# Performance work log

Hardware: AMD Instinct MI355X
Metric: run time of the kernel (lower is better)

## Reference

```python
import jax, jax.numpy as jnp
import numpy as np

BOUNDS = 1.6  # aabb = [[b,b,b],[-b,-b,-b]]
C = 72       # output_coordinate_dim per plane


def _sample_planes(grids, coords):
    """Bilinear grid_sample, align_corners=True, padding_mode='border'.
    grids:  [P, C, H, W]
    coords: [P, N, 2] with (x, y) in [-1, 1]; x indexes W, y indexes H.
    returns [P, N, C]
    """
    P, Cc, H, W = grids.shape
    x = (coords[..., 0] + 1.0) * 0.5 * (W - 1)
    y = (coords[..., 1] + 1.0) * 0.5 * (H - 1)
    # border padding: clamp the sampling coordinate to the valid range
    x = jnp.clip(x, 0.0, W - 1)
    y = jnp.clip(y, 0.0, H - 1)
    x0 = jnp.floor(x)
    y0 = jnp.floor(y)
    wx = (x - x0)[..., None]  # [P, N, 1]
    wy = (y - y0)[..., None]
    x0i = x0.astype(jnp.int32)
    y0i = y0.astype(jnp.int32)
    x1i = jnp.minimum(x0i + 1, W - 1)
    y1i = jnp.minimum(y0i + 1, H - 1)

    def one_plane(g, y0i, y1i, x0i, x1i):
        # g: [C, H, W]; index tensors: [N] -> each gather [C, N] -> [N, C]
        v00 = g[:, y0i, x0i].T
        v01 = g[:, y0i, x1i].T
        v10 = g[:, y1i, x0i].T
        v11 = g[:, y1i, x1i].T
        return v00, v01, v10, v11

    v00, v01, v10, v11 = jax.vmap(one_plane)(grids, y0i, y1i, x0i, x1i)
    top = v00 * (1.0 - wx) + v01 * wx
    bot = v10 * (1.0 - wx) + v11 * wx
    return top * (1.0 - wy) + bot * wy  # [P, N, C]


def _triplane_forward(pts, grids_list):
    N = pts.shape[0]
    # normalize_aabb with aabb = [[b,b,b],[-b,-b,-b]]
    pts_n = (pts - BOUNDS) * (2.0 / (-BOUNDS - BOUNDS)) - 1.0  # == -pts / BOUNDS
    # plane coordinate combos: (0,1), (0,2), (1,2)
    coords = jnp.stack([pts_n[:, jnp.array([0, 1])],
                        pts_n[:, jnp.array([0, 2])],
                        pts_n[:, jnp.array([1, 2])]], axis=0)  # [3, N, 2]
    feats = []
    prev = None
    for g in grids_list:  # fixed small loop over scales
        samp = _sample_planes(g, coords)                 # [3, N, C]
        tri = samp.transpose(1, 0, 2).reshape(N, 3 * C)  # concat plane feats
        prev = tri if prev is None else tri + prev       # cumulative across scales
        feats.append(prev)
    return jnp.concatenate(feats, axis=-1)  # [N, 3*C*n_scales]


def setup_inputs() -> dict:
    key = jax.random.key(0)
    ks = jax.random.split(key, 5)
    N = 100000
    pts = jax.random.normal(ks[0], (N, 3), dtype=jnp.float32)
    resos = [64, 128, 256, 512]
    grids = {}
    for i, r in enumerate(resos):
        # original init is uniform(-0.01, 0.01)
        grids[f"grids_s{i}"] = jax.random.uniform(
            ks[i + 1], (3, C, r, r), dtype=jnp.float32, minval=-0.01, maxval=0.01)
    return {"pts": pts, **grids}


def reference(pts, grids_s0, grids_s1, grids_s2, grids_s3):
    return _triplane_forward(pts, [grids_s0, grids_s1, grids_s2, grids_s3])
```

## Files before the change

kernel.cpp:

```cpp
#include <hip/hip_runtime.h>


#define TP_C 72
#define TP_PLANES 3
#define TP_SCALES 4
#define TP_INV_BOUNDS 0.625f
#define TP_CVEC (TP_C / 4)

__global__ __launch_bounds__(256) void transpose_kernel(
    const float* __restrict__ in, float* __restrict__ out, int r)
{
    __shared__ float tile[32][33];

    int xt = blockIdx.x * 32;
    int ct = blockIdx.y * 32;
    int py = blockIdx.z;
    int p  = py / r;
    int y  = py - p * r;
    int tx = threadIdx.x;
    int ty = threadIdx.y;

    const float* inp = in + ((size_t)p * TP_C) * (size_t)r * (size_t)r + (size_t)y * r;

    #pragma unroll
    for (int i = 0; i < 4; ++i) {
        int c = ct + ty + i * 8;
        if (c < TP_C) {
            tile[ty + i * 8][tx] = inp[(size_t)c * r * r + xt + tx];
        }
    }
    __syncthreads();

    float* outp = out + ((size_t)py * r) * TP_C;
    #pragma unroll
    for (int i = 0; i < 4; ++i) {
        int x = xt + ty + i * 8;
        int c = ct + tx;
        if (c < TP_C) {
            outp[(size_t)x * TP_C + c] = tile[tx][ty + i * 8];
        }
    }
}

__global__ __launch_bounds__(256) void triplane_gather_kernel(
    const float* __restrict__ pts,
    const float* __restrict__ t0,
    const float* __restrict__ t1,
    const float* __restrict__ t2,
    const float* __restrict__ t3,
    float* __restrict__ out,
    int N)
{
    int idx = blockIdx.x * blockDim.x + threadIdx.x;
    int total = N * TP_PLANES * TP_CVEC;
    if (idx >= total) return;

    int cv = idx % TP_CVEC;
    int t  = idx / TP_CVEC;
    int p  = t % TP_PLANES;
    int n  = t / TP_PLANES;

    float nx = -pts[n * 3 + 0] * TP_INV_BOUNDS;
    float ny = -pts[n * 3 + 1] * TP_INV_BOUNDS;
    float nz = -pts[n * 3 + 2] * TP_INV_BOUNDS;

    float cx, cy;
    if (p == 0)      { cx = nx; cy = ny; }
    else if (p == 1) { cx = nx; cy = nz; }
    else             { cx = ny; cy = nz; }

    const float* grids[TP_SCALES] = { t0, t1, t2, t3 };
    const int    res[TP_SCALES]   = { 64, 128, 256, 512 };

    float4 acc = make_float4(0.f, 0.f, 0.f, 0.f);
    float* outrow = out + (size_t)n * (TP_SCALES * TP_PLANES * TP_C)
                        + (size_t)p * TP_C + cv * 4;

    #pragma unroll
    for (int s = 0; s < TP_SCALES; ++s) {
        const int r = res[s];
        const float rm1 = (float)(r - 1);

        float fx = (cx + 1.0f) * 0.5f * rm1;
        float fy = (cy + 1.0f) * 0.5f * rm1;
        fx = fminf(fmaxf(fx, 0.0f), rm1);
        fy = fminf(fmaxf(fy, 0.0f), rm1);

        float x0f = floorf(fx);
        float y0f = floorf(fy);
        float wx = fx - x0f;
        float wy = fy - y0f;
        int x0 = (int)x0f;
        int y0 = (int)y0f;
        int x1 = min(x0 + 1, r - 1);
        int y1 = min(y0 + 1, r - 1);

        const float* g = grids[s] + ((size_t)p * r * r) * TP_C + (size_t)cv * 4;
        const float4* r0c0 = (const float4*)(g + ((size_t)y0 * r + x0) * TP_C);
        const float4* r0c1 = (const float4*)(g + ((size_t)y0 * r + x1) * TP_C);
        const float4* r1c0 = (const float4*)(g + ((size_t)y1 * r + x0) * TP_C);
        const float4* r1c1 = (const float4*)(g + ((size_t)y1 * r + x1) * TP_C);

        float4 v00 = *r0c0;
        float4 v01 = *r0c1;
        float4 v10 = *r1c0;
        float4 v11 = *r1c1;

        float iwx = 1.0f - wx;
        float iwy = 1.0f - wy;

        float tpx, tpy, tpz, tpw, bt;
        tpx = v00.x * iwx + v01.x * wx;
        bt  = v10.x * iwx + v11.x * wx;
        acc.x += tpx * iwy + bt * wy;
        tpy = v00.y * iwx + v01.y * wx;
        bt  = v10.y * iwx + v11.y * wx;
        acc.y += tpy * iwy + bt * wy;
        tpz = v00.z * iwx + v01.z * wx;
        bt  = v10.z * iwx + v11.z * wx;
        acc.z += tpz * iwy + bt * wy;
        tpw = v00.w * iwx + v01.w * wx;
        bt  = v10.w * iwx + v11.w * wx;
        acc.w += tpw * iwy + bt * wy;

        *(float4*)(outrow + s * (TP_PLANES * TP_C)) = acc;
    }
}

extern "C" void kernel_launch(void* const* d_in, const int* in_sizes, int n_in,
                              void* d_out, int out_size, void* d_ws, size_t ws_size,
                              hipStream_t stream) {
    const float* pts = (const float*)d_in[0];
    const float* g[TP_SCALES] = {
        (const float*)d_in[1], (const float*)d_in[2],
        (const float*)d_in[3], (const float*)d_in[4] };
    float* out = (float*)d_out;

    const int res[TP_SCALES] = { 64, 128, 256, 512 };

    float* tg[TP_SCALES];
    size_t off = 0;
    for (int s = 0; s < TP_SCALES; ++s) {
        tg[s] = (float*)d_ws + off;
        off += (size_t)TP_PLANES * TP_C * res[s] * res[s];
    }

    for (int s = 0; s < TP_SCALES; ++s) {
        int r = res[s];
        dim3 block(32, 8);
        dim3 grid(r / 32, (TP_C + 31) / 32, TP_PLANES * r);
        transpose_kernel<<<grid, block, 0, stream>>>(g[s], tg[s], r);
    }

    int N = in_sizes[0] / 3;
    int total = N * TP_PLANES * TP_CVEC;
    int block = 256;
    int grid = (total + block - 1) / block;
    triplane_gather_kernel<<<grid, block, 0, stream>>>(
        pts, tg[0], tg[1], tg[2], tg[3], out, N);
}
```

Baseline: 821.9 us.

## Merge per-scale grid transposes into one launch with float4 wide tiles

Replaces four separate transpose launches with a single kernel whose blocks index into a concatenated tile space across all scales. Each block transposes 128 pixels by 72 channels through padded shared memory, reading float4 along pixels and writing float4 contiguous channel-last rows. This is meant to cut launch overhead, the wasted threads from padding 72 channels to 96, and the narrow scalar global accesses. The larger shared-memory tile (about 37KB) may lower occupancy, and the float4 loads rely on pixel offsets staying 16-byte aligned.

```diff
diff --git a/kernel.cpp b/kernel.cpp
--- a/kernel.cpp
+++ b/kernel.cpp
@@ -7,38 +7,59 @@
 #define TP_INV_BOUNDS 0.625f
 #define TP_CVEC (TP_C / 4)
 
-__global__ __launch_bounds__(256) void transpose_kernel(
-    const float* __restrict__ in, float* __restrict__ out, int r)
+#define TP_TILES0 96
+#define TP_TILES1 480
+#define TP_TILES2 2016
+#define TP_TILES3 8160
+
+__global__ __launch_bounds__(256) void transpose_all_kernel(
+    const float* __restrict__ g0, const float* __restrict__ g1,
+    const float* __restrict__ g2, const float* __restrict__ g3,
+    float* __restrict__ t0, float* __restrict__ t1,
+    float* __restrict__ t2, float* __restrict__ t3)
 {
-    __shared__ float tile[32][33];
+    int b = blockIdx.x;
+    const float* in;
+    float* out;
+    int rr, tile;
+    if (b < TP_TILES0)      { in = g0; out = t0; rr = 64 * 64;   tile = b; }
+    else if (b < TP_TILES1) { in = g1; out = t1; rr = 128 * 128; tile = b - TP_TILES0; }
+    else if (b < TP_TILES2) { in = g2; out = t2; rr = 256 * 256; tile = b - TP_TILES1; }
+    else                    { in = g3; out = t3; rr = 512 * 512; tile = b - TP_TILES2; }
 
-    int xt = blockIdx.x * 32;
-    int ct = blockIdx.y * 32;
-    int py = blockIdx.z;
-    int p  = py / r;
-    int y  = py - p * r;
-    int tx = threadIdx.x;
-    int ty = threadIdx.y;
+    int P0  = tile * 128;
+    int p   = P0 / rr;
+    int px0 = P0 - p * rr;
 
-    const float* inp = in + ((size_t)p * TP_C) * (size_t)r * (size_t)r + (size_t)y * r;
+    __shared__ float lds[TP_C * 129];
+
+    const float* inp = in + ((size_t)p * TP_C) * (size_t)rr + px0;
+    int t = threadIdx.x;
 
     #pragma unroll
-    for (int i = 0; i < 4; ++i) {
-        int c = ct + ty + i * 8;
-        if (c < TP_C) {
-            tile[ty + i * 8][tx] = inp[(size_t)c * r * r + xt + tx];
-        }
+    for (int j = 0; j < 9; ++j) {
+        int idx = j * 256 + t;
+        int c   = idx >> 5;
+        int q4  = idx & 31;
+        float4 v = *(const float4*)(inp + (size_t)c * rr + q4 * 4);
+        float* l = lds + c * 129 + q4 * 4;
+        l[0] = v.x; l[1] = v.y; l[2] = v.z; l[3] = v.w;
     }
     __syncthreads();
 
-    float* outp = out + ((size_t)py * r) * TP_C;
+    float* outp = out + (size_t)P0 * TP_C;
     #pragma unroll
-    for (int i = 0; i < 4; ++i) {
-        int x = xt + ty + i * 8;
-        int c = ct + tx;
-        if (c < TP_C) {
-            outp[(size_t)x * TP_C + c] = tile[tx][ty + i * 8];
-        }
+    for (int j = 0; j < 9; ++j) {
+        int idx = j * 256 + t;
+        int q   = idx / 18;
+        int c4  = idx - q * 18;
+        const float* l = lds + (c4 * 4) * 129 + q;
+        float4 v;
+        v.x = l[0 * 129];
+        v.y = l[1 * 129];
+        v.z = l[2 * 129];
+        v.w = l[3 * 129];
+        *(float4*)(outp + (size_t)idx * 4) = v;
     }
 }
 
@@ -145,12 +166,8 @@
         off += (size_t)TP_PLANES * TP_C * res[s] * res[s];
     }
 
-    for (int s = 0; s < TP_SCALES; ++s) {
-        int r = res[s];
-        dim3 block(32, 8);
-        dim3 grid(r / 32, (TP_C + 31) / 32, TP_PLANES * r);
-        transpose_kernel<<<grid, block, 0, stream>>>(g[s], tg[s], r);
-    }
+    transpose_all_kernel<<<TP_TILES3, 256, 0, stream>>>(
+        g[0], g[1], g[2], g[3], tg[0], tg[1], tg[2], tg[3]);
 
     int N = in_sizes[0] / 3;
     int total = N * TP_PLANES * TP_CVEC;
```

Result: faster. 765.4 us (-6.9%).
